# Kernel optimization log

Measured on AMD Instinct MI355X. Metric: run time of the kernel, lower is better.

Reference implementation:

```python
import jax, jax.numpy as jnp
import numpy as np
import math

N_EMBD = 1024
N_HEAD = 16
BLOCK_SIZE = 2048
B, T = 2, 2048


def setup_inputs() -> dict:
    key = jax.random.key(0)
    ks = jax.random.split(key, 12)
    s = 0.02
    C = N_EMBD
    return {
        "x": jax.random.normal(ks[0], (B, T, C), dtype=jnp.float32),
        # LayerNorm 1
        "ln1_w": jnp.ones((C,), jnp.float32),
        "ln1_b": jnp.zeros((C,), jnp.float32),
        # attention: weights stored [in, out]
        "attn_w": jax.random.normal(ks[1], (C, 3 * C), dtype=jnp.float32) * s,
        "attn_b": jnp.zeros((3 * C,), jnp.float32),
        "proj_w": jax.random.normal(ks[2], (C, C), dtype=jnp.float32) * s,
        "proj_b": jnp.zeros((C,), jnp.float32),
        # LayerNorm 2
        "ln2_w": jnp.ones((C,), jnp.float32),
        "ln2_b": jnp.zeros((C,), jnp.float32),
        # MLP
        "fc_w": jax.random.normal(ks[3], (C, 4 * C), dtype=jnp.float32) * s,
        "fc_b": jnp.zeros((4 * C,), jnp.float32),
        "mlp_proj_w": jax.random.normal(ks[4], (4 * C, C), dtype=jnp.float32) * s,
        "mlp_proj_b": jnp.zeros((C,), jnp.float32),
    }


def _layernorm(x, w, b, eps=1e-5):
    mu = jnp.mean(x, axis=-1, keepdims=True)
    var = jnp.mean(jnp.square(x - mu), axis=-1, keepdims=True)
    return (x - mu) * jax.lax.rsqrt(var + eps) * w + b


def _attention(x, attn_w, attn_b, proj_w, proj_b):
    Bn, Tn, C = x.shape
    hs = C // N_HEAD
    qkv = x @ attn_w + attn_b                      # [B,T,3C]
    q, k, v = jnp.split(qkv, 3, axis=-1)
    # [B,H,T,hs]
    q = q.reshape(Bn, Tn, N_HEAD, hs).transpose(0, 2, 1, 3)
    k = k.reshape(Bn, Tn, N_HEAD, hs).transpose(0, 2, 1, 3)
    v = v.reshape(Bn, Tn, N_HEAD, hs).transpose(0, 2, 1, 3)
    att = jnp.einsum('bhqd,bhkd->bhqk', q, k) / math.sqrt(hs)  # [B,H,T,T]
    mask = jnp.tril(jnp.ones((Tn, Tn), dtype=bool))
    att = jnp.where(mask, att, -jnp.inf)
    att = jax.nn.softmax(att, axis=-1)
    y = jnp.einsum('bhqk,bhkd->bhqd', att, v)      # [B,H,T,hs]
    y = y.transpose(0, 2, 1, 3).reshape(Bn, Tn, C)
    return y @ proj_w + proj_b


def reference(x, ln1_w, ln1_b, attn_w, attn_b, proj_w, proj_b,
              ln2_w, ln2_b, fc_w, fc_b, mlp_proj_w, mlp_proj_b):
    x = x + _attention(_layernorm(x, ln1_w, ln1_b), attn_w, attn_b, proj_w, proj_b)
    h = _layernorm(x, ln2_w, ln2_b)
    h = jax.nn.gelu(h @ fc_w + fc_b, approximate=False)  # torch nn.GELU default = exact erf
    return x + (h @ mlp_proj_w + mlp_proj_b)
```

## Files before the change

### kernel.cpp

```cpp
#include <hip/hip_runtime.h>
#include <math.h>

typedef short s8x __attribute__((ext_vector_type(8)));
typedef float f32x4 __attribute__((ext_vector_type(4)));

__device__ __forceinline__ float bf2f(short u) {
    return __uint_as_float(((unsigned int)(unsigned short)u) << 16);
}
__device__ __forceinline__ short f2bf(float f) {
    unsigned int x = __float_as_uint(f);
    unsigned int r = (x + 0x7FFFu + ((x >> 16) & 1u)) >> 16;
    return (short)(unsigned short)r;
}

__device__ __forceinline__ void gl2lds16(const short* g, const short* l) {
    __builtin_amdgcn_global_load_lds(
        (const __attribute__((address_space(1))) void*)(unsigned long long)g,
        (__attribute__((address_space(3))) void*)(unsigned int)(unsigned long long)l,
        16, 0, 0);
}

__device__ __forceinline__ void ln_row(const float* __restrict__ xin,
                                       const float* __restrict__ w,
                                       const float* __restrict__ bb,
                                       short* __restrict__ out, int row, int lane) {
    const float4* xr = (const float4*)(xin + (long)row * 1024);
    float4 v[4];
    float s1 = 0.f, s2 = 0.f;
#pragma unroll
    for (int i = 0; i < 4; ++i) {
        v[i] = xr[lane + i * 64];
        s1 += v[i].x + v[i].y + v[i].z + v[i].w;
        s2 += v[i].x*v[i].x + v[i].y*v[i].y + v[i].z*v[i].z + v[i].w*v[i].w;
    }
#pragma unroll
    for (int off = 32; off > 0; off >>= 1) {
        s1 += __shfl_xor(s1, off, 64);
        s2 += __shfl_xor(s2, off, 64);
    }
    const float mu = s1 * (1.0f / 1024.0f);
    float var = s2 * (1.0f / 1024.0f) - mu * mu;
    var = fmaxf(var, 0.0f);
    const float rs = rsqrtf(var + 1e-5f);
    short4* orow = (short4*)(out + (long)row * 1024);
#pragma unroll
    for (int i = 0; i < 4; ++i) {
        const int ci = (lane + i * 64) * 4;
        const float4 wv = *(const float4*)(w + ci);
        const float4 bv = *(const float4*)(bb + ci);
        short4 o;
        o.x = f2bf((v[i].x - mu) * rs * wv.x + bv.x);
        o.y = f2bf((v[i].y - mu) * rs * wv.y + bv.y);
        o.z = f2bf((v[i].z - mu) * rs * wv.z + bv.z);
        o.w = f2bf((v[i].w - mu) * rs * wv.w + bv.w);
        orow[lane + i * 64] = o;
    }
}

__global__ __launch_bounds__(256) void ln_k(const float* __restrict__ xin,
                                            const float* __restrict__ w,
                                            const float* __restrict__ bb,
                                            short* __restrict__ out) {
    ln_row(xin, w, bb, out, blockIdx.x * 4 + (threadIdx.x >> 6), threadIdx.x & 63);
}

__global__ __launch_bounds__(256) void pre_k(
        const float* __restrict__ w0, const float* __restrict__ w1,
        const float* __restrict__ w2, const float* __restrict__ w3,
        short* __restrict__ o0, short* __restrict__ o1,
        short* __restrict__ o2, short* __restrict__ o3,
        const float* __restrict__ x, const float* __restrict__ ln1w,
        const float* __restrict__ ln1b, short* __restrict__ xln) {
    int bid = blockIdx.x;
    if (bid >= 12288) {
        ln_row(x, ln1w, ln1b, xln, (bid - 12288) * 4 + (threadIdx.x >> 6), threadIdx.x & 63);
        return;
    }
    const float* in; short* out; int K, N, nx;
    if (bid < 3072)      { in = w0; out = o0; K = 1024; N = 3072; nx = 96; }
    else if (bid < 4096) { bid -= 3072; in = w1; out = o1; K = 1024; N = 1024; nx = 32; }
    else if (bid < 8192) { bid -= 4096; in = w2; out = o2; K = 1024; N = 4096; nx = 128; }
    else                 { bid -= 8192; in = w3; out = o3; K = 4096; N = 1024; nx = 32; }
    const int n0 = (bid % nx) * 32, k0 = (bid / nx) * 32;
    __shared__ float tile[32][33];
    const int tx = threadIdx.x & 31, ty = threadIdx.x >> 5;
#pragma unroll
    for (int i = 0; i < 4; ++i) {
        const int k = ty + i * 8;
        tile[k][tx] = in[(long)(k0 + k) * N + n0 + tx];
    }
    __syncthreads();
#pragma unroll
    for (int i = 0; i < 4; ++i) {
        const int n = ty + i * 8;
        out[(long)(n0 + n) * K + k0 + tx] = f2bf(tile[tx][n]);
    }
}

template <int EPI, typename OutT>
__device__ __forceinline__ void epi_store(OutT* out, const float* resid, long oidx, float v) {
    if constexpr (EPI == 0) {
        out[oidx] = f2bf(v);
    } else if constexpr (EPI == 1) {
        const float u = v * (0.79788456080f + 0.03567740814f * v * v);
        v = v / (1.0f + __expf(-2.0f * u));
        out[oidx] = f2bf(v);
    } else {
        v += resid[oidx];
        out[oidx] = v;
    }
}

template <int EPI, typename OutT>
__global__ __launch_bounds__(256) void gemm_k(const short* __restrict__ A,
                                              const short* __restrict__ Bt,
                                              const float* __restrict__ bias,
                                              const float* __restrict__ resid,
                                              OutT* __restrict__ out,
                                              int M, int N, int K) {
    __shared__ __align__(16) short sA[2][128 * 32];
    __shared__ __align__(16) short sB[2][128 * 32];
    const int tid = threadIdx.x;
    const int lane = tid & 63, wave = tid >> 6;
    const int wr = (wave >> 1) * 64, wc = (wave & 1) * 64;
    const int lrow = lane & 15, quad = lane >> 4;
    const int bm = blockIdx.y * 128, bn = blockIdx.x * 128;
    const short* Ap = A + (long)(bm + (tid >> 2)) * K + (tid & 3) * 8;
    const short* Bp = Bt + (long)(bn + (tid >> 2)) * K + (tid & 3) * 8;
    const long rowstep = (long)64 * K;

    auto stage = [&](int p, int k0) {
        gl2lds16(Ap + k0,           sA[p] + tid * 8);
        gl2lds16(Ap + rowstep + k0, sA[p] + 2048 + tid * 8);
        gl2lds16(Bp + k0,           sB[p] + tid * 8);
        gl2lds16(Bp + rowstep + k0, sB[p] + 2048 + tid * 8);
    };

    f32x4 acc[4][4] = {};
    stage(0, 0);
    const int S = K >> 5;
    for (int s = 0; s < S; ++s) {
        const int p = s & 1;
        __syncthreads();
        if (s + 1 < S) stage(p ^ 1, (s + 1) << 5);
        const short* pA = sA[p];
        const short* pB = sB[p];
        s8x af[4], bfr[4];
#pragma unroll
        for (int i = 0; i < 4; ++i) af[i]  = *(const s8x*)(pA + (wr + i*16 + lrow) * 32 + quad * 8);
#pragma unroll
        for (int j = 0; j < 4; ++j) bfr[j] = *(const s8x*)(pB + (wc + j*16 + lrow) * 32 + quad * 8);
#pragma unroll
        for (int i = 0; i < 4; ++i)
#pragma unroll
            for (int j = 0; j < 4; ++j)
                acc[i][j] = __builtin_amdgcn_mfma_f32_16x16x32_bf16(af[i], bfr[j], acc[i][j], 0, 0, 0);
    }
#pragma unroll
    for (int i = 0; i < 4; ++i) {
#pragma unroll
        for (int j = 0; j < 4; ++j) {
#pragma unroll
            for (int r = 0; r < 4; ++r) {
                const int row = bm + wr + i*16 + quad*4 + r;
                const int col = bn + wc + j*16 + lrow;
                epi_store<EPI>(out, resid, (long)row * N + col, acc[i][j][r] + bias[col]);
            }
        }
    }
}

template <int EPI, typename OutT>
__global__ __launch_bounds__(256) void gemm64_k(const short* __restrict__ A,
                                                const short* __restrict__ Bt,
                                                const float* __restrict__ bias,
                                                const float* __restrict__ resid,
                                                OutT* __restrict__ out,
                                                int M, int N, int K) {
    __shared__ __align__(16) short sA[2][2][64 * 32];
    __shared__ __align__(16) short sB[2][2][128 * 32];
    const int tid = threadIdx.x;
    const int lane = tid & 63, wave = tid >> 6;
    const int lrow = lane & 15, quad = lane >> 4;
    const int bm = blockIdx.y * 64, bn = blockIdx.x * 128;
    const short* Ap = A + (long)(bm + (tid >> 2)) * K + (tid & 3) * 8;
    const short* Bp = Bt + (long)(bn + (tid >> 2)) * K + (tid & 3) * 8;
    const long rowstep = (long)64 * K;

    auto stage = [&](int p, int k0) {
#pragma unroll
        for (int hp = 0; hp < 2; ++hp) {
            gl2lds16(Ap + k0 + hp * 32,           sA[p][hp] + tid * 8);
            gl2lds16(Bp + k0 + hp * 32,           sB[p][hp] + tid * 8);
            gl2lds16(Bp + rowstep + k0 + hp * 32, sB[p][hp] + 2048 + tid * 8);
        }
    };

    f32x4 acc[8] = {};
    stage(0, 0);
    const int S = K >> 6;
    for (int s = 0; s < S; ++s) {
        const int p = s & 1;
        __syncthreads();
        if (s + 1 < S) stage(p ^ 1, (s + 1) << 6);
#pragma unroll
        for (int hp = 0; hp < 2; ++hp) {
            const s8x af = *(const s8x*)(sA[p][hp] + (wave * 16 + lrow) * 32 + quad * 8);
#pragma unroll
            for (int j = 0; j < 8; ++j) {
                const s8x bf = *(const s8x*)(sB[p][hp] + (j * 16 + lrow) * 32 + quad * 8);
                acc[j] = __builtin_amdgcn_mfma_f32_16x16x32_bf16(af, bf, acc[j], 0, 0, 0);
            }
        }
    }
#pragma unroll
    for (int j = 0; j < 8; ++j) {
#pragma unroll
        for (int r = 0; r < 4; ++r) {
            const int row = bm + wave * 16 + quad * 4 + r;
            const int col = bn + j * 16 + lrow;
            epi_store<EPI>(out, resid, (long)row * N + col, acc[j][r] + bias[col]);
        }
    }
}

#define ATT_CS (0.125f * 1.4426950408889634f)
#define ATT_C0 (14.426950408889634f)

__global__ __launch_bounds__(256) void attn_k(const short* __restrict__ qkv,
                                              short* __restrict__ y) {
    const int bx = blockIdx.x;
    const int b = blockIdx.y >> 4, h = blockIdx.y & 15;
    const int qtA = bx, qtB = 31 - bx;
    const int tid = threadIdx.x, lane = tid & 63, wave = tid >> 6;
    const int lrow = lane & 15, quad = lane >> 4;
    const long base = (long)b * 2048 * 3072;

    __shared__ __align__(16) short sK[2][64 * 64];
    __shared__ __align__(16) short sVt[2][64 * 64];

    s8x qfA0, qfA1, qfB0, qfB1;
    {
        const short* qpA = qkv + base + (long)(qtA * 64 + wave * 16 + lrow) * 3072 + h * 64 + quad * 8;
        qfA0 = *(const s8x*)qpA; qfA1 = *(const s8x*)(qpA + 32);
        const short* qpB = qkv + base + (long)(qtB * 64 + wave * 16 + lrow) * 3072 + h * 64 + quad * 8;
        qfB0 = *(const s8x*)qpB; qfB1 = *(const s8x*)(qpB + 32);
    }
    f32x4 oA[4], oB[4];
    float lA = 0.f, lB = 0.f;
#pragma unroll
    for (int d = 0; d < 4; ++d) { oA[d] = f32x4{0.f,0.f,0.f,0.f}; oB[d] = f32x4{0.f,0.f,0.f,0.f}; }

    const int srow = tid >> 3, sg = tid & 7;
    const int sw0 = ((srow & 7) ^ (srow >> 3)) & 7;
    const int sw1 = (((srow + 32) & 7) ^ ((srow + 32) >> 3)) & 7;
    const short* kbase = qkv + base + 1024 + h * 64;
    const short* vbase = qkv + base + 2048 + h * 64;

    uint4 vr0, vr1;
    auto issueK = [&](int p, int k0) {
        gl2lds16(kbase + (long)(k0 + srow) * 3072      + (sg ^ sw0) * 8, sK[p] + tid * 8);
        gl2lds16(kbase + (long)(k0 + srow + 32) * 3072 + (sg ^ sw1) * 8, sK[p] + 2048 + tid * 8);
    };
    auto loadV = [&](int k0) {
        const short* vp = vbase + (long)(k0 + srow) * 3072 + sg * 8;
        vr0 = *(const uint4*)vp;
        vr1 = *(const uint4*)(vp + 32 * 3072);
    };
    auto writeV = [&](int p) {
        const short* e0 = (const short*)&vr0;
        const short* e1 = (const short*)&vr1;
#pragma unroll
        for (int i = 0; i < 8; ++i) {
            const int d = sg * 8 + i;
            const int swd = i ^ sg;
            sVt[p][d * 64 + ( srow       ^ (swd << 3))] = e0[i];
            sVt[p][d * 64 + ((srow + 32) ^ (swd << 3))] = e1[i];
        }
    };

    auto tile_step = [&](const s8x& qf0, const s8x& qf1, const s8x* kf0, const s8x* kf1,
                         const short* pV, f32x4* o, float& lsum, int qt, int kt, int k0) {
        f32x4 s[4];
        __builtin_amdgcn_s_setprio(1);
#pragma unroll
        for (int ct = 0; ct < 4; ++ct) {
            f32x4 t = f32x4{0.f, 0.f, 0.f, 0.f};
            t = __builtin_amdgcn_mfma_f32_16x16x32_bf16(kf0[ct], qf0, t, 0, 0, 0);
            t = __builtin_amdgcn_mfma_f32_16x16x32_bf16(kf1[ct], qf1, t, 0, 0, 0);
            s[ct] = t;
        }
        __builtin_amdgcn_s_setprio(0);
        const int qrow = qt * 64 + wave * 16 + lrow;
        float pv[4][4];
        if (kt == qt) {
#pragma unroll
            for (int ct = 0; ct < 4; ++ct)
#pragma unroll
                for (int r = 0; r < 4; ++r) {
                    const int key = k0 + ct * 16 + quad * 4 + r;
                    const float pp = exp2f(fmaf(s[ct][r], ATT_CS, -ATT_C0));
                    const float pt = __uint_as_float(__float_as_uint(pp) & 0xFFFF0000u);
                    pv[ct][r] = (key > qrow) ? 0.f : pt;
                }
        } else {
#pragma unroll
            for (int ct = 0; ct < 4; ++ct)
#pragma unroll
                for (int r = 0; r < 4; ++r) {
                    const float pp = exp2f(fmaf(s[ct][r], ATT_CS, -ATT_C0));
                    pv[ct][r] = __uint_as_float(__float_as_uint(pp) & 0xFFFF0000u);
                }
        }
#pragma unroll
        for (int ct = 0; ct < 4; ++ct)
            lsum += (pv[ct][0] + pv[ct][1]) + (pv[ct][2] + pv[ct][3]);

        unsigned int w2[4][2];
#pragma unroll
        for (int ct = 0; ct < 4; ++ct)
#pragma unroll
            for (int p2 = 0; p2 < 2; ++p2)
                w2[ct][p2] = __builtin_amdgcn_perm(__float_as_uint(pv[ct][2 * p2 + 1]),
                                                   __float_as_uint(pv[ct][2 * p2]), 0x07060302u);
        s8x pa[2];
#pragma unroll
        for (int ks = 0; ks < 2; ++ks) {
            auto rAC = __builtin_amdgcn_permlane32_swap((int)w2[2 * ks][0], (int)w2[2 * ks + 1][0], false, false);
            auto rBD = __builtin_amdgcn_permlane32_swap((int)w2[2 * ks][1], (int)w2[2 * ks + 1][1], false, false);
            auto mAC = __builtin_amdgcn_permlane16_swap(rAC[0], rAC[1], false, false);
            auto mBD = __builtin_amdgcn_permlane16_swap(rBD[0], rBD[1], false, false);
            int4 f;
            f.x = mAC[0]; f.y = mBD[0]; f.z = mAC[1]; f.w = mBD[1];
            pa[ks] = *(const s8x*)&f;
        }
        __builtin_amdgcn_s_setprio(1);
#pragma unroll
        for (int ks = 0; ks < 2; ++ks) {
#pragma unroll
            for (int dt = 0; dt < 4; ++dt) {
                const int d = dt * 16 + lrow;
                const int swd = ((d & 7) ^ (d >> 3)) & 7;
                const s8x vf = *(const s8x*)(pV + d * 64 + (((ks * 4 + quad) ^ swd) * 8));
                o[dt] = __builtin_amdgcn_mfma_f32_16x16x32_bf16(pa[ks], vf, o[dt], 0, 0, 0);
            }
        }
        __builtin_amdgcn_s_setprio(0);
    };

    issueK(0, 0);
    loadV(0);
    for (int kt = 0; kt <= qtB; ++kt) {
        const int p = kt & 1, k0 = kt * 64;
        writeV(p);
        __syncthreads();
        if (kt < qtB) { issueK(p ^ 1, k0 + 64); loadV(k0 + 64); }

        s8x kf0[4], kf1[4];
#pragma unroll
        for (int ct = 0; ct < 4; ++ct) {
            const int row = ct * 16 + lrow;
            const int swr = ((row & 7) ^ (row >> 3)) & 7;
            kf0[ct] = *(const s8x*)(sK[p] + row * 64 + ((quad ^ swr) * 8));
            kf1[ct] = *(const s8x*)(sK[p] + row * 64 + (((4 + quad) ^ swr) * 8));
        }
        if (kt <= qtA) tile_step(qfA0, qfA1, kf0, kf1, sVt[p], oA, lA, qtA, kt, k0);
        tile_step(qfB0, qfB1, kf0, kf1, sVt[p], oB, lB, qtB, kt, k0);
    }

    lA += __shfl_xor(lA, 16, 64); lA += __shfl_xor(lA, 32, 64);
    lB += __shfl_xor(lB, 16, 64); lB += __shfl_xor(lB, 32, 64);
    float rA[4], rB[4];
#pragma unroll
    for (int r = 0; r < 4; ++r) {
        rA[r] = 1.0f / __shfl(lA, quad * 4 + r, 64);
        rB[r] = 1.0f / __shfl(lB, quad * 4 + r, 64);
    }
#pragma unroll
    for (int dt = 0; dt < 4; ++dt) {
#pragma unroll
        for (int r = 0; r < 4; ++r) {
            const int qA = qtA * 64 + wave * 16 + quad * 4 + r;
            const int qB = qtB * 64 + wave * 16 + quad * 4 + r;
            y[((long)b * 2048 + qA) * 1024 + h * 64 + dt * 16 + lrow] = f2bf(oA[dt][r] * rA[r]);
            y[((long)b * 2048 + qB) * 1024 + h * 64 + dt * 16 + lrow] = f2bf(oB[dt][r] * rB[r]);
        }
    }
}

extern "C" void kernel_launch(void* const* d_in, const int* in_sizes, int n_in,
                              void* d_out, int out_size, void* d_ws, size_t ws_size,
                              hipStream_t stream) {
    const float* x      = (const float*)d_in[0];
    const float* ln1_w  = (const float*)d_in[1];
    const float* ln1_b  = (const float*)d_in[2];
    const float* attn_w = (const float*)d_in[3];
    const float* attn_b = (const float*)d_in[4];
    const float* proj_w = (const float*)d_in[5];
    const float* proj_b = (const float*)d_in[6];
    const float* ln2_w  = (const float*)d_in[7];
    const float* ln2_b  = (const float*)d_in[8];
    const float* fc_w   = (const float*)d_in[9];
    const float* fc_b   = (const float*)d_in[10];
    const float* mlp_w  = (const float*)d_in[11];
    const float* mlp_b  = (const float*)d_in[12];

    char* ws = (char*)d_ws;
    short* attn_wt = (short*)(ws + 0);
    short* proj_wt = (short*)(ws + 6291456L);
    short* fc_wt   = (short*)(ws + 8388608L);
    short* mlp_wt  = (short*)(ws + 16777216L);
    short* slotA   = (short*)(ws + 25165824L);
    short* slotB   = (short*)(ws + 33554432L);

    short* xln  = slotA;
    short* yb   = slotA;
    short* hb   = slotA;
    short* qkvb = slotB;
    short* hh   = slotB;
    float* x1   = (float*)d_out;
    float* outp = (float*)d_out;

    pre_k<<<13312, 256, 0, stream>>>(attn_w, proj_w, fc_w, mlp_w,
                                     attn_wt, proj_wt, fc_wt, mlp_wt,
                                     x, ln1_w, ln1_b, xln);

    gemm_k<0, short><<<dim3(24, 32), 256, 0, stream>>>(xln, attn_wt, attn_b, nullptr, qkvb, 4096, 3072, 1024);
    attn_k<<<dim3(16, 32), 256, 0, stream>>>(qkvb, yb);
    gemm64_k<2, float><<<dim3(8, 64), 256, 0, stream>>>(yb, proj_wt, proj_b, x, x1, 4096, 1024, 1024);
    ln_k<<<1024, 256, 0, stream>>>(x1, ln2_w, ln2_b, hb);
    gemm_k<1, short><<<dim3(32, 32), 256, 0, stream>>>(hb, fc_wt, fc_b, nullptr, hh, 4096, 4096, 1024);
    gemm64_k<3, float><<<dim3(8, 64), 256, 0, stream>>>(hh, mlp_wt, mlp_b, x1, outp, 4096, 1024, 4096);
}
```

Measured before the change: 343.6 us.

## Load V tiles directly to LDS and use transpose reads for PV fragments

```diff
diff --git a/kernel.cpp b/kernel.cpp
--- a/kernel.cpp
+++ b/kernel.cpp
@@ -3,6 +3,7 @@
 
 typedef short s8x __attribute__((ext_vector_type(8)));
 typedef float f32x4 __attribute__((ext_vector_type(4)));
+typedef int   i32x2 __attribute__((ext_vector_type(2)));
 
 __device__ __forceinline__ float bf2f(short u) {
     return __uint_as_float(((unsigned int)(unsigned short)u) << 16);
@@ -227,6 +228,9 @@
 #define ATT_CS (0.125f * 1.4426950408889634f)
 #define ATT_C0 (14.426950408889634f)
 
+#define TR16(dst, off) \
+    asm volatile("ds_read_b64_tr_b16 %0, %1 offset:" off : "=v"(dst) : "v"(tva))
+
 __global__ __launch_bounds__(256) void attn_k(const short* __restrict__ qkv,
                                               short* __restrict__ y) {
     const int bx = blockIdx.x;
@@ -237,7 +241,7 @@
     const long base = (long)b * 2048 * 3072;
 
     __shared__ __align__(16) short sK[2][64 * 64];
-    __shared__ __align__(16) short sVt[2][64 * 64];
+    __shared__ __align__(16) short sV[2][4096];
 
     s8x qfA0, qfA1, qfB0, qfB1;
     {
@@ -255,34 +259,25 @@
     const int sw0 = ((srow & 7) ^ (srow >> 3)) & 7;
     const int sw1 = (((srow + 32) & 7) ^ ((srow + 32) >> 3)) & 7;
     const short* kbase = qkv + base + 1024 + h * 64;
-    const short* vbase = qkv + base + 2048 + h * 64;
-
-    uint4 vr0, vr1;
     auto issueK = [&](int p, int k0) {
         gl2lds16(kbase + (long)(k0 + srow) * 3072      + (sg ^ sw0) * 8, sK[p] + tid * 8);
         gl2lds16(kbase + (long)(k0 + srow + 32) * 3072 + (sg ^ sw1) * 8, sK[p] + 2048 + tid * 8);
     };
-    auto loadV = [&](int k0) {
-        const short* vp = vbase + (long)(k0 + srow) * 3072 + sg * 8;
-        vr0 = *(const uint4*)vp;
-        vr1 = *(const uint4*)(vp + 32 * 3072);
+
+    const int vslot   = (tid >> 3) & 7;
+    const int vkbl    = 2 * (vslot & 3) + (vslot >> 2);
+    const int vklocal = vkbl * 4 + ((tid >> 1) & 3);
+    const short* vsrc = qkv + base + 2048 + h * 64
+                      + (long)vklocal * 3072 + wave * 16 + 8 * (tid & 1);
+    auto issueV = [&](int p, int k0) {
+        gl2lds16(vsrc + (long)k0 * 3072,        sV[p] + tid * 8);
+        gl2lds16(vsrc + (long)(k0 + 32) * 3072, sV[p] + 2048 + tid * 8);
     };
-    auto writeV = [&](int p) {
-        const short* e0 = (const short*)&vr0;
-        const short* e1 = (const short*)&vr1;
-#pragma unroll
-        for (int i = 0; i < 8; ++i) {
-            const int d = sg * 8 + i;
-            const int swd = i ^ sg;
-            sVt[p][d * 64 + ( srow       ^ (swd << 3))] = e0[i];
-            sVt[p][d * 64 + ((srow + 32) ^ (swd << 3))] = e1[i];
-        }
-    };
+    const unsigned trb = (unsigned)(unsigned long long)(&sV[0][0]) + (unsigned)lane * 8u;
 
     auto tile_step = [&](const s8x& qf0, const s8x& qf1, const s8x* kf0, const s8x* kf1,
-                         const short* pV, f32x4* o, float& lsum, int qt, int kt, int k0) {
+                         const s8x (*vfr)[4], f32x4* o, float& lsum, int qt, int kt, int k0) {
         f32x4 s[4];
-        __builtin_amdgcn_s_setprio(1);
 #pragma unroll
         for (int ct = 0; ct < 4; ++ct) {
             f32x4 t = f32x4{0.f, 0.f, 0.f, 0.f};
@@ -290,7 +285,6 @@
             t = __builtin_amdgcn_mfma_f32_16x16x32_bf16(kf1[ct], qf1, t, 0, 0, 0);
             s[ct] = t;
         }
-        __builtin_amdgcn_s_setprio(0);
         const int qrow = qt * 64 + wave * 16 + lrow;
         float pv[4][4];
         if (kt == qt) {
@@ -334,27 +328,19 @@
             f.x = mAC[0]; f.y = mBD[0]; f.z = mAC[1]; f.w = mBD[1];
             pa[ks] = *(const s8x*)&f;
         }
-        __builtin_amdgcn_s_setprio(1);
-#pragma unroll
-        for (int ks = 0; ks < 2; ++ks) {
-#pragma unroll
-            for (int dt = 0; dt < 4; ++dt) {
-                const int d = dt * 16 + lrow;
-                const int swd = ((d & 7) ^ (d >> 3)) & 7;
-                const s8x vf = *(const s8x*)(pV + d * 64 + (((ks * 4 + quad) ^ swd) * 8));
-                o[dt] = __builtin_amdgcn_mfma_f32_16x16x32_bf16(pa[ks], vf, o[dt], 0, 0, 0);
-            }
-        }
-        __builtin_amdgcn_s_setprio(0);
+#pragma unroll
+        for (int ks = 0; ks < 2; ++ks)
+#pragma unroll
+            for (int dt = 0; dt < 4; ++dt)
+                o[dt] = __builtin_amdgcn_mfma_f32_16x16x32_bf16(pa[ks], vfr[ks][dt], o[dt], 0, 0, 0);
     };
 
     issueK(0, 0);
-    loadV(0);
+    issueV(0, 0);
     for (int kt = 0; kt <= qtB; ++kt) {
         const int p = kt & 1, k0 = kt * 64;
-        writeV(p);
         __syncthreads();
-        if (kt < qtB) { issueK(p ^ 1, k0 + 64); loadV(k0 + 64); }
+        if (kt < qtB) { issueK(p ^ 1, k0 + 64); issueV(p ^ 1, k0 + 64); }
 
         s8x kf0[4], kf1[4];
 #pragma unroll
@@ -364,8 +350,33 @@
             kf0[ct] = *(const s8x*)(sK[p] + row * 64 + ((quad ^ swr) * 8));
             kf1[ct] = *(const s8x*)(sK[p] + row * 64 + (((4 + quad) ^ swr) * 8));
         }
-        if (kt <= qtA) tile_step(qfA0, qfA1, kf0, kf1, sVt[p], oA, lA, qtA, kt, k0);
-        tile_step(qfB0, qfB1, kf0, kf1, sVt[p], oB, lB, qtB, kt, k0);
+
+        const unsigned tva = trb + (unsigned)(p << 13);
+        i32x2 tr[16];
+        TR16(tr[0],  "0");    TR16(tr[1],  "512");
+        TR16(tr[2],  "1024"); TR16(tr[3],  "1536");
+        TR16(tr[4],  "2048"); TR16(tr[5],  "2560");
+        TR16(tr[6],  "3072"); TR16(tr[7],  "3584");
+        TR16(tr[8],  "4096"); TR16(tr[9],  "4608");
+        TR16(tr[10], "5120"); TR16(tr[11], "5632");
+        TR16(tr[12], "6144"); TR16(tr[13], "6656");
+        TR16(tr[14], "7168"); TR16(tr[15], "7680");
+        asm volatile("s_waitcnt lgkmcnt(0)" ::: "memory");
+        __builtin_amdgcn_sched_barrier(0);
+        s8x vfr[2][4];
+#pragma unroll
+        for (int ks = 0; ks < 2; ++ks)
+#pragma unroll
+            for (int dt = 0; dt < 4; ++dt) {
+                const int i2 = ks * 8 + dt * 2;
+                int4 f;
+                f.x = tr[i2][0]; f.y = tr[i2][1];
+                f.z = tr[i2 + 1][0]; f.w = tr[i2 + 1][1];
+                vfr[ks][dt] = *(const s8x*)&f;
+            }
+
+        if (kt <= qtA) tile_step(qfA0, qfA1, kf0, kf1, vfr, oA, lA, qtA, kt, k0);
+        tile_step(qfB0, qfB1, kf0, kf1, vfr, oB, lB, qtB, kt, k0);
     }
 
     lA += __shfl_xor(lA, 16, 64); lA += __shfl_xor(lA, 32, 64);
```

After: 332.6 us. -3.2%, faster.
